# Kernel optimization log

Hardware: AMD Instinct MI355X
Metric: run time of the kernel (lower is better)

The kernel has to match this reference:

```python
import jax, jax.numpy as jnp
import numpy as np

N_NODES = 50000
N_EDGES = 800000
D = 128
BN_EPS = 1e-5


def setup_inputs() -> dict:
    key = jax.random.key(0)
    ks = jax.random.split(key, 12)
    inp = {
        "X": jax.random.normal(ks[0], (N_NODES, D), dtype=jnp.float32),
        "W_A": jax.random.normal(ks[1], (D, D), dtype=jnp.float32) * 0.05,
        "b_A": jax.random.normal(ks[2], (D,), dtype=jnp.float32) * 0.05,
        "W_B": jax.random.normal(ks[3], (D, D), dtype=jnp.float32) * 0.05,
        "b_B": jax.random.normal(ks[4], (D,), dtype=jnp.float32) * 0.05,
        "W_D": jax.random.normal(ks[5], (D, D), dtype=jnp.float32) * 0.05,
        "b_D": jax.random.normal(ks[6], (D,), dtype=jnp.float32) * 0.05,
        "W_E": jax.random.normal(ks[7], (D, D), dtype=jnp.float32) * 0.05,
        "b_E": jax.random.normal(ks[8], (D,), dtype=jnp.float32) * 0.05,
        "gamma": jnp.ones((D,), dtype=jnp.float32),
        "beta": jnp.zeros((D,), dtype=jnp.float32),
        "src": jax.random.randint(ks[9], (N_EDGES,), 0, N_NODES, dtype=jnp.int64 if jax.config.jax_enable_x64 else jnp.int32),
        "dst": jax.random.randint(ks[10], (N_EDGES,), 0, N_NODES, dtype=jnp.int64 if jax.config.jax_enable_x64 else jnp.int32),
    }
    return inp


def reference(X, W_A, b_A, W_B, b_B, W_D, b_D, W_E, b_E, gamma, beta, src, dst):
    n = X.shape[0]
    # Node projections (nn.Linear: x @ W^T + b; here W stored as [d_in, d_out])
    AX = X @ W_A + b_A
    BX = X @ W_B + b_B
    DX = X @ W_D + b_D
    EX = X @ W_E + b_E

    # Per-edge gate: e_j = DX[src] + EX[dst]; sigma = sigmoid(e_j)
    sigma = jax.nn.sigmoid(DX[src] + EX[dst])  # [E, D]

    # Weighted segment-sum aggregation onto destination nodes
    num = jax.ops.segment_sum(sigma * BX[src], dst, num_segments=n)  # [N, D]
    den = jax.ops.segment_sum(sigma, dst, num_segments=n)            # [N, D]
    deg = jax.ops.segment_sum(jnp.ones_like(dst, dtype=X.dtype), dst, num_segments=n)  # [N]

    has_msg = (deg > 0)[:, None]
    den_safe = jnp.where(has_msg, den, 1.0)
    # DGL: nodes with no incoming messages keep H = X
    H = jnp.where(has_msg, AX + num / den_safe, X)

    # snorm scaling
    H = H * (1.0 / n)

    # BatchNorm1d over node dim (training-mode batch statistics, biased var)
    mean = jnp.mean(H, axis=0)
    var = jnp.mean(jnp.square(H - mean), axis=0)
    H = (H - mean) / jnp.sqrt(var + BN_EPS) * gamma + beta

    H = jax.nn.relu(H)
    return X + H
```

## Files before the change

### kernel.cpp

```cpp
#include <hip/hip_runtime.h>
#include <hip/hip_bf16.h>
#include <math.h>

#define NN 50000
#define DD 128
#define BN_EPS 1e-5f
#define PADN 53248
#define GEMM_BLOCKS 782
#define NBUCKET 32

typedef short short8 __attribute__((ext_vector_type(8)));
typedef float f32x4 __attribute__((ext_vector_type(4)));

__device__ __forceinline__ unsigned short f2bf(float f) {
    __hip_bfloat16 h = __float2bfloat16(f);
    return *reinterpret_cast<unsigned short*>(&h);
}
__device__ __forceinline__ float frcp(float x) { return __builtin_amdgcn_rcpf(x); }

__global__ __launch_bounds__(256) void prep_w(
    const float* __restrict__ W0, const float* __restrict__ W1,
    const float* __restrict__ W2, const float* __restrict__ W3,
    unsigned short* __restrict__ Wt, int* __restrict__ deg,
    float* __restrict__ acc2)
{
    const int b = blockIdx.x;
    if (b >= 4) {
        const int zb = b - 4;
        const int idx = zb * 256 + threadIdx.x;
        if (idx < PADN / 4) ((int4*)deg)[idx] = make_int4(0, 0, 0, 0);
        if (zb == 0) {
            #pragma unroll
            for (int j = 0; j < 8; ++j)
                ((float4*)acc2)[j * 256 + threadIdx.x] =
                    make_float4(0.f, 0.f, 0.f, 0.f);
        }
        return;
    }
    const int which = b;
    const float* W = (which == 0) ? W0 : (which == 1) ? W1 : (which == 2) ? W2 : W3;
    unsigned short* O = Wt + (size_t)which * 16384;
    for (int it = 0; it < 8; ++it) {
        const int id = it * 256 + threadIdx.x;
        const int col = id >> 4;
        const int kc  = id & 15;
        unsigned int pk[4];
        #pragma unroll
        for (int p = 0; p < 4; ++p) {
            const float f0 = W[(kc * 8 + p * 2 + 0) * DD + col];
            const float f1 = W[(kc * 8 + p * 2 + 1) * DD + col];
            pk[p] = (unsigned int)f2bf(f0) | ((unsigned int)f2bf(f1) << 16);
        }
        uint4 v = make_uint4(pk[0], pk[1], pk[2], pk[3]);
        *(uint4*)(O + col * 128 + kc * 8) = v;
    }
}

__global__ __launch_bounds__(512, 4) void gemm4_scatter(
    const float* __restrict__ X, const unsigned short* __restrict__ Wt,
    const float* __restrict__ bA, const float* __restrict__ bB,
    const float* __restrict__ bD, const float* __restrict__ bE,
    float* __restrict__ AX, float* __restrict__ QX,
    unsigned short* __restrict__ BD,
    const int* __restrict__ src, const int* __restrict__ dst,
    int* __restrict__ cursor, int* __restrict__ srt, int ne)
{
    if (blockIdx.x >= GEMM_BLOCKS) {
        const int e = (blockIdx.x - GEMM_BLOCKS) * 512 + threadIdx.x;
        if (e < ne) {
            const int p = atomicAdd(&cursor[dst[e]], 1);
            srt[p] = src[e];
        }
        return;
    }

    __shared__ char xs[64 * 256];
    const int row0 = blockIdx.x * 64;
    const int tid  = threadIdx.x;

    #pragma unroll
    for (int it = 0; it < 2; ++it) {
        const int idx = it * 512 + tid;
        const int r = idx >> 4;
        const int c = idx & 15;
        const bool valid = (row0 + r) < NN;
        float4 va = make_float4(0.f, 0.f, 0.f, 0.f);
        float4 vb = make_float4(0.f, 0.f, 0.f, 0.f);
        if (valid) {
            const float* gp = X + (size_t)(row0 + r) * DD + c * 8;
            va = *(const float4*)(gp);
            vb = *(const float4*)(gp + 4);
        }
        uint4 pk;
        pk.x = (unsigned int)f2bf(va.x) | ((unsigned int)f2bf(va.y) << 16);
        pk.y = (unsigned int)f2bf(va.z) | ((unsigned int)f2bf(va.w) << 16);
        pk.z = (unsigned int)f2bf(vb.x) | ((unsigned int)f2bf(vb.y) << 16);
        pk.w = (unsigned int)f2bf(vb.z) | ((unsigned int)f2bf(vb.w) << 16);
        *(uint4*)(xs + r * 256 + ((c * 16) ^ ((r & 7) << 4))) = pk;
    }
    __syncthreads();

    const int wid  = tid >> 6;
    const int p    = wid >> 1;
    const int h    = wid & 1;
    const int lane = tid & 63;
    const int lr = lane & 15, lg = lane >> 4;

    f32x4 acc[4][4];
    #pragma unroll
    for (int m = 0; m < 4; ++m)
        #pragma unroll
        for (int n = 0; n < 4; ++n)
            acc[m][n] = (f32x4){0.f, 0.f, 0.f, 0.f};

    const char* wb = (const char*)(Wt + (size_t)p * 16384) + h * 64 * 256;

    #pragma unroll
    for (int k = 0; k < 4; ++k) {
        short8 aW[4];
        #pragma unroll
        for (int n = 0; n < 4; ++n)
            aW[n] = *(const short8*)(wb + (n * 16 + lr) * 256 + k * 64 + lg * 16);
        short8 bX[4];
        #pragma unroll
        for (int m = 0; m < 4; ++m)
            bX[m] = *(const short8*)(xs + (m * 16 + lr) * 256 +
                                     ((k * 64 + lg * 16) ^ ((lr & 7) << 4)));
        #pragma unroll
        for (int m = 0; m < 4; ++m)
            #pragma unroll
            for (int n = 0; n < 4; ++n)
                acc[m][n] = __builtin_amdgcn_mfma_f32_16x16x32_bf16(
                    aW[n], bX[m], acc[m][n], 0, 0, 0);
    }

    const float* bias = (p == 0) ? bA : (p == 1) ? bB : (p == 2) ? bD : bE;
    #pragma unroll
    for (int n = 0; n < 4; ++n) {
        const int cbase = h * 64 + n * 16 + lg * 4;
        const float4 bv = *(const float4*)(bias + cbase);
        #pragma unroll
        for (int m = 0; m < 4; ++m) {
            const int row = row0 + m * 16 + lr;
            if (row < NN) {
                float v0 = acc[m][n][0] + bv.x;
                float v1 = acc[m][n][1] + bv.y;
                float v2 = acc[m][n][2] + bv.z;
                float v3 = acc[m][n][3] + bv.w;
                if (p == 0) {
                    *(float4*)(AX + (size_t)row * DD + cbase) = make_float4(v0, v1, v2, v3);
                } else if (p == 3) {
                    *(float4*)(QX + (size_t)row * DD + cbase) =
                        make_float4(__expf(-v0), __expf(-v1), __expf(-v2), __expf(-v3));
                } else {
                    if (p == 2) {
                        v0 = __expf(-v0); v1 = __expf(-v1);
                        v2 = __expf(-v2); v3 = __expf(-v3);
                    }
                    uint2 pk;
                    pk.x = (unsigned int)f2bf(v0) | ((unsigned int)f2bf(v1) << 16);
                    pk.y = (unsigned int)f2bf(v2) | ((unsigned int)f2bf(v3) << 16);
                    char* dstp = (char*)BD + (size_t)row * 512 + (cbase >> 2) * 16
                               + ((p == 2) ? 8 : 0);
                    *(uint2*)dstp = pk;
                }
            }
        }
    }
}

__global__ void hist_k(const int* __restrict__ dst, int* __restrict__ deg, int ne)
{
    const int e = blockIdx.x * blockDim.x + threadIdx.x;
    if (e < ne) atomicAdd(&deg[dst[e]], 1);
}

__global__ __launch_bounds__(1024) void scan_k(const int* __restrict__ deg,
                                               int* __restrict__ off,
                                               int* __restrict__ cursor)
{
    __shared__ int ws[16];
    const int t = threadIdx.x;
    int4 v[13];
    const int4* dp = (const int4*)deg + t * 13;
    #pragma unroll
    for (int j = 0; j < 13; ++j) v[j] = dp[j];

    int s = 0;
    #pragma unroll
    for (int j = 0; j < 13; ++j) s += v[j].x + v[j].y + v[j].z + v[j].w;

    int incl = s;
    #pragma unroll
    for (int o = 1; o < 64; o <<= 1) {
        const int u = __shfl_up(incl, o, 64);
        if ((t & 63) >= o) incl += u;
    }
    if ((t & 63) == 63) ws[t >> 6] = incl;
    __syncthreads();
    int wbase = 0;
    for (int i = 0; i < (t >> 6); ++i) wbase += ws[i];

    int run = wbase + incl - s;
    int4* op = (int4*)off + t * 13;
    int4* cp = (int4*)cursor + t * 13;
    #pragma unroll
    for (int j = 0; j < 13; ++j) {
        int4 w;
        w.x = run; run += v[j].x;
        w.y = run; run += v[j].y;
        w.z = run; run += v[j].z;
        w.w = run; run += v[j].w;
        op[j] = w;
        cp[j] = w;
    }
}

__global__ __launch_bounds__(256) void agg_bn_k(
    const float* __restrict__ AX, const float* __restrict__ QX,
    const uint4* __restrict__ BD4, const float* __restrict__ X,
    const int* __restrict__ off, const int* __restrict__ srt,
    float* __restrict__ H, float* __restrict__ acc2)
{
    const int wid  = threadIdx.x >> 6;
    const int lane = threadIdx.x & 63;
    const int half = lane >> 5;
    const int f    = lane & 31;
    const int node = blockIdx.x * 4 + wid;
    const int beg = off[node], end = off[node + 1];

    const float4 q = *(const float4*)(QX + (size_t)node * DD + f * 4);
    float num[4] = {0.f, 0.f, 0.f, 0.f};
    float den[4] = {0.f, 0.f, 0.f, 0.f};

#define EDGE4(wv)                                                            \
    {                                                                        \
        const float b0_ = __uint_as_float((wv).x << 16);                     \
        const float b1_ = __uint_as_float((wv).x & 0xffff0000u);             \
        const float b2_ = __uint_as_float((wv).y << 16);                     \
        const float b3_ = __uint_as_float((wv).y & 0xffff0000u);             \
        const float p0_ = __uint_as_float((wv).z << 16);                     \
        const float p1_ = __uint_as_float((wv).z & 0xffff0000u);             \
        const float p2_ = __uint_as_float((wv).w << 16);                     \
        const float p3_ = __uint_as_float((wv).w & 0xffff0000u);             \
        const float g0_ = frcp(fmaf(p0_, q.x, 1.0f));                        \
        const float g1_ = frcp(fmaf(p1_, q.y, 1.0f));                        \
        const float g2_ = frcp(fmaf(p2_, q.z, 1.0f));                        \
        const float g3_ = frcp(fmaf(p3_, q.w, 1.0f));                        \
        num[0] = fmaf(g0_, b0_, num[0]); den[0] += g0_;                      \
        num[1] = fmaf(g1_, b1_, num[1]); den[1] += g1_;                      \
        num[2] = fmaf(g2_, b2_, num[2]); den[2] += g2_;                      \
        num[3] = fmaf(g3_, b3_, num[3]); den[3] += g3_;                      \
    }

    int i = beg;
    for (; i + 8 <= end; i += 8) {
        int ss[4];
        #pragma unroll
        for (int u = 0; u < 4; ++u) ss[u] = srt[i + 2 * u + half];
        uint4 wv[4];
        #pragma unroll
        for (int u = 0; u < 4; ++u) wv[u] = BD4[(size_t)ss[u] * 32 + f];
        #pragma unroll
        for (int u = 0; u < 4; ++u) EDGE4(wv[u]);
    }
    for (; i + 2 <= end; i += 2) {
        const int s = srt[i + half];
        const uint4 wv = BD4[(size_t)s * 32 + f];
        EDGE4(wv);
    }
    if (i < end && half == 0) {
        const int s = srt[i];
        const uint4 wv = BD4[(size_t)s * 32 + f];
        EDGE4(wv);
    }
#undef EDGE4

    #pragma unroll
    for (int j = 0; j < 4; ++j) {
        num[j] += __shfl_xor(num[j], 32);
        den[j] += __shfl_xor(den[j], 32);
    }

    float4 hv = make_float4(0.f, 0.f, 0.f, 0.f);
    if (half == 0) {
        if (end > beg) {
            const float4 ax = *(const float4*)(AX + (size_t)node * DD + f * 4);
            hv.x = ax.x + num[0] * frcp(den[0]);
            hv.y = ax.y + num[1] * frcp(den[1]);
            hv.z = ax.z + num[2] * frcp(den[2]);
            hv.w = ax.w + num[3] * frcp(den[3]);
        } else {
            hv = *(const float4*)(X + (size_t)node * DD + f * 4);
        }
        hv.x *= (1.0f / NN); hv.y *= (1.0f / NN);
        hv.z *= (1.0f / NN); hv.w *= (1.0f / NN);
        *(float4*)(H + (size_t)node * DD + f * 4) = hv;
    }

    __shared__ float red1[4][32][4], red2[4][32][4];
    if (half == 0) {
        red1[wid][f][0] = hv.x; red2[wid][f][0] = hv.x * hv.x;
        red1[wid][f][1] = hv.y; red2[wid][f][1] = hv.y * hv.y;
        red1[wid][f][2] = hv.z; red2[wid][f][2] = hv.z * hv.z;
        red1[wid][f][3] = hv.w; red2[wid][f][3] = hv.w * hv.w;
    }
    __syncthreads();
    const int t = threadIdx.x;
    if (t < 128) {
        const int ff = t >> 2, cc = t & 3;
        const float a1 = red1[0][ff][cc] + red1[1][ff][cc]
                       + red1[2][ff][cc] + red1[3][ff][cc];
        const float a2 = red2[0][ff][cc] + red2[1][ff][cc]
                       + red2[2][ff][cc] + red2[3][ff][cc];
        float* bucket = acc2 + (size_t)(blockIdx.x & (NBUCKET - 1)) * 256;
        atomicAdd(&bucket[t], a1);
        atomicAdd(&bucket[128 + t], a2);
    }
}

__global__ __launch_bounds__(256) void final_k(
    const float* __restrict__ H, const float* __restrict__ X,
    const float* __restrict__ acc2,
    const float* __restrict__ gamma, const float* __restrict__ beta,
    float* __restrict__ out)
{
    __shared__ float stat[256];
    const int t = threadIdx.x;
    {
        float s = 0.f;
        #pragma unroll
        for (int k = 0; k < NBUCKET; ++k) s += acc2[k * 256 + t];
        stat[t] = s;
    }
    __syncthreads();

    #pragma unroll
    for (int it = 0; it < 8; ++it) {
        const int i = (blockIdx.x * 8 + it) * 256 + t;
        if (i >= NN * 32) return;
        const int f = (i & 31) * 4;
        const float4 h = *(const float4*)(H + (size_t)i * 4);
        const float4 x = *(const float4*)(X + (size_t)i * 4);
        float4 o;
        #pragma unroll
        for (int c = 0; c < 4; ++c) {
            const float mean = stat[f + c] * (1.0f / NN);
            const float var  = stat[128 + f + c] * (1.0f / NN) - mean * mean;
            const float rstd = rsqrtf(var + BN_EPS);
            const float hv = (c == 0) ? h.x : (c == 1) ? h.y : (c == 2) ? h.z : h.w;
            const float xv = (c == 0) ? x.x : (c == 1) ? x.y : (c == 2) ? x.z : x.w;
            float v = (hv - mean) * rstd * gamma[f + c] + beta[f + c];
            v = fmaxf(v, 0.f);
            const float r = xv + v;
            if (c == 0) o.x = r; else if (c == 1) o.y = r; else if (c == 2) o.z = r; else o.w = r;
        }
        *(float4*)(out + (size_t)i * 4) = o;
    }
}

extern "C" void kernel_launch(void* const* d_in, const int* in_sizes, int n_in,
                              void* d_out, int out_size, void* d_ws, size_t ws_size,
                              hipStream_t stream)
{
    const float* X     = (const float*)d_in[0];
    const float* W_A   = (const float*)d_in[1];
    const float* b_A   = (const float*)d_in[2];
    const float* W_B   = (const float*)d_in[3];
    const float* b_B   = (const float*)d_in[4];
    const float* W_D   = (const float*)d_in[5];
    const float* b_D   = (const float*)d_in[6];
    const float* W_E   = (const float*)d_in[7];
    const float* b_E   = (const float*)d_in[8];
    const float* gamma = (const float*)d_in[9];
    const float* beta  = (const float*)d_in[10];
    const int*   src   = (const int*)d_in[11];
    const int*   dst   = (const int*)d_in[12];
    const int    ne    = in_sizes[11];
    float* out = (float*)d_out;

    char* w = (char*)d_ws;
    const size_t ndf = (size_t)NN * DD * sizeof(float);
    unsigned short* Wt = (unsigned short*)w;  w += 4 * 16384 * sizeof(unsigned short);
    float* AX = (float*)w;                    w += ndf;
    float* QX = (float*)w;                    w += ndf;
    unsigned short* BD = (unsigned short*)w;  w += (size_t)NN * 256 * sizeof(unsigned short);
    float* H  = (float*)w;                    w += ndf;
    float* acc2 = (float*)w;                  w += NBUCKET * 256 * sizeof(float);
    int* deg    = (int*)w;                    w += (size_t)PADN * sizeof(int);
    int* off    = (int*)w;                    w += (size_t)PADN * sizeof(int);
    int* cursor = (int*)w;                    w += (size_t)PADN * sizeof(int);
    int* srt    = (int*)w;                    w += (size_t)ne * sizeof(int);

    prep_w<<<60, 256, 0, stream>>>(W_A, W_B, W_D, W_E, Wt, deg, acc2);

    hist_k<<<(ne + 255) / 256, 256, 0, stream>>>(dst, deg, ne);
    scan_k<<<1, 1024, 0, stream>>>(deg, off, cursor);

    const int sc_blocks = (ne + 511) / 512;
    gemm4_scatter<<<GEMM_BLOCKS + sc_blocks, 512, 0, stream>>>(
        X, Wt, b_A, b_B, b_D, b_E, AX, QX, BD, src, dst, cursor, srt, ne);

    agg_bn_k<<<NN / 4, 256, 0, stream>>>(AX, QX, (const uint4*)BD, X, off, srt, H, acc2);

    final_k<<<(NN * 32 + 2047) / 2048, 256, 0, stream>>>(H, X, acc2, gamma, beta, out);
}
```

Baseline: 303.8 us.

## Process two 64-row tiles per GEMM block with register prefetch; scatter blocks first

Each GEMM block now handles 128 rows in two 64-row tiles, prefetching the second tile's X rows into registers while the first tile's MFMAs run, then reusing the same shared buffer. Scatter blocks are moved to the front of the grid so the edge bucketing dispatches before the GEMM work. This halves GEMM block count and overlaps global loads with compute, at the cost of more registers per thread and an extra barrier.

```diff
diff --git a/kernel.cpp b/kernel.cpp
--- a/kernel.cpp
+++ b/kernel.cpp
@@ -6,7 +6,7 @@
 #define DD 128
 #define BN_EPS 1e-5f
 #define PADN 53248
-#define GEMM_BLOCKS 782
+#define GEMM_BLOCKS2 391
 #define NBUCKET 32
 
 typedef short short8 __attribute__((ext_vector_type(8)));
@@ -56,64 +56,18 @@
     }
 }
 
-__global__ __launch_bounds__(512, 4) void gemm4_scatter(
-    const float* __restrict__ X, const unsigned short* __restrict__ Wt,
-    const float* __restrict__ bA, const float* __restrict__ bB,
-    const float* __restrict__ bD, const float* __restrict__ bE,
+__device__ __forceinline__ void gemm_tile(
+    const char* xs, const char* wb, int p, int h, int lr, int lg,
+    int rowbase, const float* __restrict__ bias,
     float* __restrict__ AX, float* __restrict__ QX,
-    unsigned short* __restrict__ BD,
-    const int* __restrict__ src, const int* __restrict__ dst,
-    int* __restrict__ cursor, int* __restrict__ srt, int ne)
-{
-    if (blockIdx.x >= GEMM_BLOCKS) {
-        const int e = (blockIdx.x - GEMM_BLOCKS) * 512 + threadIdx.x;
-        if (e < ne) {
-            const int p = atomicAdd(&cursor[dst[e]], 1);
-            srt[p] = src[e];
-        }
-        return;
-    }
-
-    __shared__ char xs[64 * 256];
-    const int row0 = blockIdx.x * 64;
-    const int tid  = threadIdx.x;
-
-    #pragma unroll
-    for (int it = 0; it < 2; ++it) {
-        const int idx = it * 512 + tid;
-        const int r = idx >> 4;
-        const int c = idx & 15;
-        const bool valid = (row0 + r) < NN;
-        float4 va = make_float4(0.f, 0.f, 0.f, 0.f);
-        float4 vb = make_float4(0.f, 0.f, 0.f, 0.f);
-        if (valid) {
-            const float* gp = X + (size_t)(row0 + r) * DD + c * 8;
-            va = *(const float4*)(gp);
-            vb = *(const float4*)(gp + 4);
-        }
-        uint4 pk;
-        pk.x = (unsigned int)f2bf(va.x) | ((unsigned int)f2bf(va.y) << 16);
-        pk.y = (unsigned int)f2bf(va.z) | ((unsigned int)f2bf(va.w) << 16);
-        pk.z = (unsigned int)f2bf(vb.x) | ((unsigned int)f2bf(vb.y) << 16);
-        pk.w = (unsigned int)f2bf(vb.z) | ((unsigned int)f2bf(vb.w) << 16);
-        *(uint4*)(xs + r * 256 + ((c * 16) ^ ((r & 7) << 4))) = pk;
-    }
-    __syncthreads();
-
-    const int wid  = tid >> 6;
-    const int p    = wid >> 1;
-    const int h    = wid & 1;
-    const int lane = tid & 63;
-    const int lr = lane & 15, lg = lane >> 4;
-
+    unsigned short* __restrict__ BD)
+{
     f32x4 acc[4][4];
     #pragma unroll
     for (int m = 0; m < 4; ++m)
         #pragma unroll
         for (int n = 0; n < 4; ++n)
             acc[m][n] = (f32x4){0.f, 0.f, 0.f, 0.f};
-
-    const char* wb = (const char*)(Wt + (size_t)p * 16384) + h * 64 * 256;
 
     #pragma unroll
     for (int k = 0; k < 4; ++k) {
@@ -134,14 +88,13 @@
                     aW[n], bX[m], acc[m][n], 0, 0, 0);
     }
 
-    const float* bias = (p == 0) ? bA : (p == 1) ? bB : (p == 2) ? bD : bE;
     #pragma unroll
     for (int n = 0; n < 4; ++n) {
         const int cbase = h * 64 + n * 16 + lg * 4;
         const float4 bv = *(const float4*)(bias + cbase);
         #pragma unroll
         for (int m = 0; m < 4; ++m) {
-            const int row = row0 + m * 16 + lr;
+            const int row = rowbase + m * 16 + lr;
             if (row < NN) {
                 float v0 = acc[m][n][0] + bv.x;
                 float v1 = acc[m][n][1] + bv.y;
@@ -169,6 +122,83 @@
     }
 }
 
+__global__ __launch_bounds__(512, 4) void gemm4_scatter(
+    const float* __restrict__ X, const unsigned short* __restrict__ Wt,
+    const float* __restrict__ bA, const float* __restrict__ bB,
+    const float* __restrict__ bD, const float* __restrict__ bE,
+    float* __restrict__ AX, float* __restrict__ QX,
+    unsigned short* __restrict__ BD,
+    const int* __restrict__ src, const int* __restrict__ dst,
+    int* __restrict__ cursor, int* __restrict__ srt, int ne)
+{
+    const int scb = (ne + 511) >> 9;
+    if (blockIdx.x < scb) {
+        const int e = blockIdx.x * 512 + threadIdx.x;
+        if (e < ne) {
+            const int p = atomicAdd(&cursor[dst[e]], 1);
+            srt[p] = src[e];
+        }
+        return;
+    }
+
+    __shared__ char xs[64 * 256];
+    const int gb   = blockIdx.x - scb;
+    const int row0 = gb * 128;
+    const int tid  = threadIdx.x;
+    const int r0 = tid >> 4;
+    const int c0 = tid & 15;
+
+#define LDROW(row, va, vb)                                                   \
+    {                                                                        \
+        if ((row) < NN) {                                                    \
+            const float* gp = X + (size_t)(row) * DD + c0 * 8;               \
+            va = *(const float4*)(gp);                                       \
+            vb = *(const float4*)(gp + 4);                                   \
+        } else {                                                             \
+            va = make_float4(0.f, 0.f, 0.f, 0.f);                           \
+            vb = make_float4(0.f, 0.f, 0.f, 0.f);                           \
+        }                                                                    \
+    }
+#define CVTSTORE(r, va, vb)                                                  \
+    {                                                                        \
+        uint4 pk;                                                            \
+        pk.x = (unsigned int)f2bf(va.x) | ((unsigned int)f2bf(va.y) << 16);  \
+        pk.y = (unsigned int)f2bf(va.z) | ((unsigned int)f2bf(va.w) << 16);  \
+        pk.z = (unsigned int)f2bf(vb.x) | ((unsigned int)f2bf(vb.y) << 16);  \
+        pk.w = (unsigned int)f2bf(vb.z) | ((unsigned int)f2bf(vb.w) << 16);  \
+        *(uint4*)(xs + (r) * 256 + ((c0 * 16) ^ (((r) & 7) << 4))) = pk;     \
+    }
+
+    float4 va0, vb0, va1, vb1;
+    LDROW(row0 + r0, va0, vb0);
+    LDROW(row0 + r0 + 32, va1, vb1);
+    CVTSTORE(r0, va0, vb0);
+    CVTSTORE(r0 + 32, va1, vb1);
+    __syncthreads();
+
+    const int wid  = tid >> 6;
+    const int p    = wid >> 1;
+    const int h    = wid & 1;
+    const int lane = tid & 63;
+    const int lr = lane & 15, lg = lane >> 4;
+    const char* wb = (const char*)(Wt + (size_t)p * 16384) + h * 64 * 256;
+    const float* bias = (p == 0) ? bA : (p == 1) ? bB : (p == 2) ? bD : bE;
+
+    LDROW(row0 + 64 + r0, va0, vb0);
+    LDROW(row0 + 64 + r0 + 32, va1, vb1);
+
+    gemm_tile(xs, wb, p, h, lr, lg, row0, bias, AX, QX, BD);
+    __syncthreads();
+
+    CVTSTORE(r0, va0, vb0);
+    CVTSTORE(r0 + 32, va1, vb1);
+    __syncthreads();
+
+    gemm_tile(xs, wb, p, h, lr, lg, row0 + 64, bias, AX, QX, BD);
+#undef LDROW
+#undef CVTSTORE
+}
+
 __global__ void hist_k(const int* __restrict__ dst, int* __restrict__ deg, int ne)
 {
     const int e = blockIdx.x * blockDim.x + threadIdx.x;
@@ -398,7 +428,7 @@
     scan_k<<<1, 1024, 0, stream>>>(deg, off, cursor);
 
     const int sc_blocks = (ne + 511) / 512;
-    gemm4_scatter<<<GEMM_BLOCKS + sc_blocks, 512, 0, stream>>>(
+    gemm4_scatter<<<sc_blocks + GEMM_BLOCKS2, 512, 0, stream>>>(
         X, Wt, b_A, b_B, b_D, b_E, AX, QX, BD, src, dst, cursor, srt, ne);
 
     agg_bn_k<<<NN / 4, 256, 0, stream>>>(AX, QX, (const uint4*)BD, X, off, srt, H, acc2);
```

Result: slower. 345.3 us (+13.6%).
